# Kernel tuning notes

Hardware: AMD Instinct MI355X
Metric: run time of the kernel (lower is better)

## Reference

```python
import jax, jax.numpy as jnp
import numpy as np

N_INPUT = 1024
HIDDEN_SIZES = [16, 16]
N_LABELS = 8
BATCH = 4096


def setup_inputs() -> dict:
    key = jax.random.key(0)
    k_x, k_w0, k_w1, k_wf = jax.random.split(key, 4)
    x = jax.random.normal(k_x, (BATCH, N_INPUT), dtype=jnp.float32)
    # per-feature MLP weights, matching nn.Parameter(torch.randn(...)) shapes
    w0 = jax.random.normal(k_w0, (N_INPUT, 1, HIDDEN_SIZES[0]), dtype=jnp.float32)
    w1 = jax.random.normal(k_w1, (N_INPUT, HIDDEN_SIZES[0], HIDDEN_SIZES[1]), dtype=jnp.float32)
    wf = jax.random.normal(k_wf, (N_INPUT, HIDDEN_SIZES[1], N_LABELS), dtype=jnp.float32)
    return {"x": x, "w0": w0, "w1": w1, "wf": wf}


def reference(x, w0, w1, wf):
    # x: [B, N] -> [B, N, 1, 1]; broadcast batched matmul against [N, k, h]
    h = x[:, :, None, None]                 # [B, N, 1, 1]
    h = jnp.tanh(jnp.matmul(h, w0))         # [B, N, 1, h0]
    h = jnp.tanh(jnp.matmul(h, w1))         # [B, N, 1, h1]
    return jnp.matmul(h, wf)                # [B, N, 1, n_labels]
```

## Files before the change

kernel.cpp:

```cpp
#include <hip/hip_runtime.h>


typedef _Float16 half4 __attribute__((ext_vector_type(4)));
typedef float f32x4 __attribute__((ext_vector_type(4)));

__device__ __forceinline__ float fast_tanh(float x) {
  float e = __builtin_amdgcn_exp2f(x * 2.885390081777927f);
  return 1.0f - 2.0f * __builtin_amdgcn_rcpf(e + 1.0f);
}

__global__ __launch_bounds__(256) void transpose_x(const float* __restrict__ src,
                                                   float* __restrict__ dst) {
  __shared__ float tile[64][65];
  const int t = threadIdx.x;
  const int bx = blockIdx.x & 15;
  const int by = blockIdx.x >> 4;
  const int c0 = bx * 64, r0 = by * 64;
  const int tr = t >> 4;
  const int tc = (t & 15) * 4;
#pragma unroll
  for (int q = 0; q < 4; ++q) {
    const float4 v = *(const float4*)(src + (size_t)(r0 + tr + q * 16) * 1024 + c0 + tc);
    tile[tr + q * 16][tc + 0] = v.x;
    tile[tr + q * 16][tc + 1] = v.y;
    tile[tr + q * 16][tc + 2] = v.z;
    tile[tr + q * 16][tc + 3] = v.w;
  }
  __syncthreads();
#pragma unroll
  for (int q = 0; q < 4; ++q) {
    const int c = tr + q * 16;
    float4 v;
    v.x = tile[tc + 0][c];
    v.y = tile[tc + 1][c];
    v.z = tile[tc + 2][c];
    v.w = tile[tc + 3][c];
    *(float4*)(dst + (size_t)(c0 + c) * 4096 + r0 + tc) = v;
  }
}

#define OBPITCH 34

__global__ __launch_bounds__(256, 8) void mlp_main(const float* __restrict__ xsrc,
                                                   const float* __restrict__ w0,
                                                   const float* __restrict__ w1,
                                                   const float* __restrict__ wf,
                                                   float* __restrict__ out,
                                                   int transposed) {
  const int tid = threadIdx.x;
  const int wid = tid >> 6;
  const int lane = tid & 63;
  const int g = lane >> 4;
  const int r = lane & 15;
  const int ig = blockIdx.x & 255;
  const int bs = blockIdx.x >> 8;
  const int i = ig * 4 + wid;
  const int bbase = bs * 512;

  __shared__ float outbuf[2][16 * OBPITCH];

  half4 aw1;
  {
    const float* w1p = w1 + i * 256 + g * 64 + r;
#pragma unroll
    for (int ii = 0; ii < 4; ++ii) aw1[ii] = (_Float16)w1p[ii * 16];
  }
  half4 awf;
  {
    const float* wfp = wf + i * 128 + g * 32 + r;
#pragma unroll
    for (int ii = 0; ii < 4; ++ii)
      awf[ii] = (r < 8) ? (_Float16)wfp[ii * 8] : (_Float16)0.0f;
  }
  float w0g[4];
  {
    const float4 v = *(const float4*)(w0 + i * 16 + g * 4);
    w0g[0] = v.x; w0g[1] = v.y; w0g[2] = v.z; w0g[3] = v.w;
  }

  const float* xp = transposed ? xsrc + (size_t)i * 4096 + bbase + r
                               : xsrc + (size_t)(bbase + r) * 1024 + i;
  const size_t xstep = transposed ? 16u : 16u * 1024u;

  const f32x4 zero = {0.f, 0.f, 0.f, 0.f};
  const int row = tid >> 4;
  const int cc = (tid & 15) * 2;

  float xv = xp[0];
  for (int t = 0; t < 32; ++t) {
    const int b0 = bbase + t * 16;
    half4 bh1;
#pragma unroll
    for (int ii = 0; ii < 4; ++ii) bh1[ii] = (_Float16)fast_tanh(xv * w0g[ii]);
    if (t < 31) xv = xp[(size_t)(t + 1) * xstep];

    f32x4 d1 = __builtin_amdgcn_mfma_f32_16x16x16f16(aw1, bh1, zero, 0, 0, 0);
    half4 bh2;
#pragma unroll
    for (int ii = 0; ii < 4; ++ii) bh2[ii] = (_Float16)fast_tanh(d1[ii]);
    f32x4 d2 = __builtin_amdgcn_mfma_f32_16x16x16f16(awf, bh2, zero, 0, 0, 0);

    float* ob = outbuf[t & 1];
    if (g < 2) {
#pragma unroll
      for (int ii = 0; ii < 4; ++ii)
        ob[r * OBPITCH + wid * 8 + g * 4 + ii] = d2[ii];
    }
    __syncthreads();
    {
      const float2 v = *(const float2*)&ob[row * OBPITCH + cc];
      *(float2*)(out + (size_t)(b0 + row) * 8192 + ig * 32 + cc) = v;
    }
  }
}

extern "C" void kernel_launch(void* const* d_in, const int* in_sizes, int n_in,
                              void* d_out, int out_size, void* d_ws, size_t ws_size,
                              hipStream_t stream) {
  const float* x = (const float*)d_in[0];
  const float* w0 = (const float*)d_in[1];
  const float* w1 = (const float*)d_in[2];
  const float* wf = (const float*)d_in[3];
  float* out = (float*)d_out;
  float* xT = (float*)d_ws;

  const size_t xT_bytes = (size_t)1024 * 4096 * sizeof(float);
  const bool useT = ws_size >= xT_bytes;
  if (useT) {
    transpose_x<<<1024, 256, 0, stream>>>(x, xT);
    mlp_main<<<2048, 256, 0, stream>>>(xT, w0, w1, wf, out, 1);
  } else {
    mlp_main<<<2048, 256, 0, stream>>>(x, w0, w1, wf, out, 0);
  }
}
```

Baseline: 169.4 us.

## Drop x transpose pre-pass and LDS output staging; store MFMA results directly

Removes the separate transpose kernel and its workspace round trip. The main kernel now reads x directly with row-strided loads. It also drops the shared-memory double buffer and per-iteration __syncthreads, so each lane writes its MFMA output fragment as a 16-byte vector store straight to global memory. The loop gets an unroll-by-2 hint. The trade-off is less coalesced x reads, which now depend on L2 reuse across neighbouring blocks, and narrower per-lane output store patterns.

After: 210.5 us. 24.2% more time.

```diff
diff --git a/kernel.cpp b/kernel.cpp
--- a/kernel.cpp
+++ b/kernel.cpp
@@ -9,44 +9,11 @@
   return 1.0f - 2.0f * __builtin_amdgcn_rcpf(e + 1.0f);
 }
 
-__global__ __launch_bounds__(256) void transpose_x(const float* __restrict__ src,
-                                                   float* __restrict__ dst) {
-  __shared__ float tile[64][65];
-  const int t = threadIdx.x;
-  const int bx = blockIdx.x & 15;
-  const int by = blockIdx.x >> 4;
-  const int c0 = bx * 64, r0 = by * 64;
-  const int tr = t >> 4;
-  const int tc = (t & 15) * 4;
-#pragma unroll
-  for (int q = 0; q < 4; ++q) {
-    const float4 v = *(const float4*)(src + (size_t)(r0 + tr + q * 16) * 1024 + c0 + tc);
-    tile[tr + q * 16][tc + 0] = v.x;
-    tile[tr + q * 16][tc + 1] = v.y;
-    tile[tr + q * 16][tc + 2] = v.z;
-    tile[tr + q * 16][tc + 3] = v.w;
-  }
-  __syncthreads();
-#pragma unroll
-  for (int q = 0; q < 4; ++q) {
-    const int c = tr + q * 16;
-    float4 v;
-    v.x = tile[tc + 0][c];
-    v.y = tile[tc + 1][c];
-    v.z = tile[tc + 2][c];
-    v.w = tile[tc + 3][c];
-    *(float4*)(dst + (size_t)(c0 + c) * 4096 + r0 + tc) = v;
-  }
-}
-
-#define OBPITCH 34
-
-__global__ __launch_bounds__(256, 8) void mlp_main(const float* __restrict__ xsrc,
-                                                   const float* __restrict__ w0,
-                                                   const float* __restrict__ w1,
-                                                   const float* __restrict__ wf,
-                                                   float* __restrict__ out,
-                                                   int transposed) {
+__global__ __launch_bounds__(256) void mlp_fused(const float* __restrict__ x,
+                                                 const float* __restrict__ w0,
+                                                 const float* __restrict__ w1,
+                                                 const float* __restrict__ wf,
+                                                 float* __restrict__ out) {
   const int tid = threadIdx.x;
   const int wid = tid >> 6;
   const int lane = tid & 63;
@@ -56,8 +23,6 @@
   const int bs = blockIdx.x >> 8;
   const int i = ig * 4 + wid;
   const int bbase = bs * 512;
-
-  __shared__ float outbuf[2][16 * OBPITCH];
 
   half4 aw1;
   {
@@ -78,21 +43,19 @@
     w0g[0] = v.x; w0g[1] = v.y; w0g[2] = v.z; w0g[3] = v.w;
   }
 
-  const float* xp = transposed ? xsrc + (size_t)i * 4096 + bbase + r
-                               : xsrc + (size_t)(bbase + r) * 1024 + i;
-  const size_t xstep = transposed ? 16u : 16u * 1024u;
+  const float* xp = x + (size_t)(bbase + r) * 1024 + i;
+  float* op = out + (size_t)(bbase + r) * 8192 + i * 8 + g * 4;
 
   const f32x4 zero = {0.f, 0.f, 0.f, 0.f};
-  const int row = tid >> 4;
-  const int cc = (tid & 15) * 2;
+  const bool do_store = (g < 2);
 
   float xv = xp[0];
+#pragma unroll 2
   for (int t = 0; t < 32; ++t) {
-    const int b0 = bbase + t * 16;
     half4 bh1;
 #pragma unroll
     for (int ii = 0; ii < 4; ++ii) bh1[ii] = (_Float16)fast_tanh(xv * w0g[ii]);
-    if (t < 31) xv = xp[(size_t)(t + 1) * xstep];
+    if (t < 31) xv = xp[(size_t)(t + 1) * 16 * 1024];
 
     f32x4 d1 = __builtin_amdgcn_mfma_f32_16x16x16f16(aw1, bh1, zero, 0, 0, 0);
     half4 bh2;
@@ -100,17 +63,7 @@
     for (int ii = 0; ii < 4; ++ii) bh2[ii] = (_Float16)fast_tanh(d1[ii]);
     f32x4 d2 = __builtin_amdgcn_mfma_f32_16x16x16f16(awf, bh2, zero, 0, 0, 0);
 
-    float* ob = outbuf[t & 1];
-    if (g < 2) {
-#pragma unroll
-      for (int ii = 0; ii < 4; ++ii)
-        ob[r * OBPITCH + wid * 8 + g * 4 + ii] = d2[ii];
-    }
-    __syncthreads();
-    {
-      const float2 v = *(const float2*)&ob[row * OBPITCH + cc];
-      *(float2*)(out + (size_t)(b0 + row) * 8192 + ig * 32 + cc) = v;
-    }
+    if (do_store) *(f32x4*)(op + (size_t)t * 16 * 8192) = d2;
   }
 }
 
@@ -122,14 +75,6 @@
   const float* w1 = (const float*)d_in[2];
   const float* wf = (const float*)d_in[3];
   float* out = (float*)d_out;
-  float* xT = (float*)d_ws;
-
-  const size_t xT_bytes = (size_t)1024 * 4096 * sizeof(float);
-  const bool useT = ws_size >= xT_bytes;
-  if (useT) {
-    transpose_x<<<1024, 256, 0, stream>>>(x, xT);
-    mlp_main<<<2048, 256, 0, stream>>>(xT, w0, w1, wf, out, 1);
-  } else {
-    mlp_main<<<2048, 256, 0, stream>>>(x, w0, w1, wf, out, 0);
-  }
+  (void)d_ws; (void)ws_size;
+  mlp_fused<<<2048, 256, 0, stream>>>(x, w0, w1, wf, out);
 }
```
